# Kernel optimization log

Hardware: AMD Instinct MI355X
Metric: run time of the kernel (lower is better)

The kernel has to match this reference:

```python
import jax, jax.numpy as jnp
import numpy as np

N = 40000   # nodes
E = 600000  # edges
G = 64      # graphs
DIN = 128   # input feature dim
H = 128     # hidden_channels
L = 3       # num_layers


def setup_inputs() -> dict:
    key = jax.random.key(0)
    ks = jax.random.split(key, 16)
    s = 0.05
    inp = {}
    inp["x"] = jax.random.normal(ks[0], (N, DIN), jnp.float32)
    inp["edge_attr"] = jax.random.normal(ks[1], (E,), jnp.float32)
    inp["node_w"] = jax.random.normal(ks[2], (DIN, H), jnp.float32) * s
    inp["node_b"] = jnp.zeros((H,), jnp.float32)
    inp["edge_w"] = jax.random.normal(ks[3], (1, H), jnp.float32) * s
    inp["edge_b"] = jnp.zeros((H,), jnp.float32)
    inp["t"] = jnp.ones((L,), jnp.float32)  # learn_t init 1.0
    inp["lin1_w"] = jax.random.normal(ks[4], (L, H, 2 * H), jnp.float32) * s
    inp["lin1_b"] = jnp.zeros((L, 2 * H), jnp.float32)
    inp["ln1_g"] = jnp.ones((L, 2 * H), jnp.float32)
    inp["ln1_bt"] = jnp.zeros((L, 2 * H), jnp.float32)
    inp["lin2_w"] = jax.random.normal(ks[5], (L, 2 * H, H), jnp.float32) * s
    inp["lin2_b"] = jnp.zeros((L, H), jnp.float32)
    inp["blk_g"] = jnp.ones((L, H), jnp.float32)
    inp["blk_b"] = jnp.zeros((L, H), jnp.float32)
    inp["hw1"] = jax.random.normal(ks[6], (H, H // 2), jnp.float32) * s
    inp["hb1"] = jnp.zeros((H // 2,), jnp.float32)
    inp["hw2"] = jax.random.normal(ks[7], (H // 2, H // 4), jnp.float32) * s
    inp["hb2"] = jnp.zeros((H // 4,), jnp.float32)
    inp["hw3"] = jax.random.normal(ks[8], (H // 4, 1), jnp.float32) * s
    inp["hb3"] = jnp.zeros((1,), jnp.float32)
    inp["edge_index"] = jax.random.randint(ks[9], (2, E), 0, N, jnp.int32)
    inp["batch"] = jnp.sort(jax.random.randint(ks[10], (N,), 0, G, jnp.int32))
    return inp


def _layer_norm(v, g, b):
    mu = jnp.mean(v, axis=-1, keepdims=True)
    var = jnp.var(v, axis=-1, keepdims=True)
    return (v - mu) * jax.lax.rsqrt(var + 1e-5) * g + b


def reference(x, edge_attr, node_w, node_b, edge_w, edge_b, t,
              lin1_w, lin1_b, ln1_g, ln1_bt, lin2_w, lin2_b,
              blk_g, blk_b, hw1, hb1, hw2, hb2, hw3, hb3,
              edge_index, batch):
    src, dst = edge_index[0], edge_index[1]
    h = x @ node_w + node_b                       # [N, H]
    ea = edge_attr[:, None] @ edge_w + edge_b     # [E, H]

    def genconv(xn, i):
        # message: relu(x_j + e) + eps
        msg = jax.nn.relu(xn[src] + ea) + 1e-7    # [E, H]
        # scatter-softmax over dst with learnable temperature t
        logit = msg * t[i]
        m = jax.ops.segment_max(logit, dst, num_segments=N)
        m = jnp.where(jnp.isfinite(m), m, 0.0)    # isolated nodes
        ex = jnp.exp(logit - m[dst])
        den = jax.ops.segment_sum(ex, dst, num_segments=N)
        agg = jax.ops.segment_sum(ex * msg, dst, num_segments=N) / jnp.maximum(den, 1e-16)
        o = agg + xn                              # add root
        # GENConv MLP: Linear(H,2H) -> LayerNorm -> ReLU -> Linear(2H,H)
        o = jax.nn.relu(_layer_norm(o @ lin1_w[i] + lin1_b[i], ln1_g[i], ln1_bt[i]))
        return o @ lin2_w[i] + lin2_b[i]

    # layer 0: bare conv (as in the torch forward)
    h = genconv(h, 0)
    # layers 1..L-1: DeepGCNLayer res+ (norm -> act -> [dropout=id in eval] -> conv -> residual)
    for i in range(1, L):
        r = jax.nn.relu(_layer_norm(h, blk_g[i], blk_b[i]))
        h = h + genconv(r, i)
    # final norm+act uses layer 0's norm/act
    h = jax.nn.relu(_layer_norm(h, blk_g[0], blk_b[0]))
    # global mean pool over graphs
    cnt = jax.ops.segment_sum(jnp.ones((N,), h.dtype), batch, num_segments=G)
    pooled = jax.ops.segment_sum(h, batch, num_segments=G) / jnp.maximum(cnt, 1.0)[:, None]
    # MLP head (dropout = identity in eval)
    o = jax.nn.relu(pooled @ hw1 + hb1)
    o = jax.nn.relu(o @ hw2 + hb2)
    return o @ hw3 + hb3                          # [G, 1]
```

## Files before the change

kernel.cpp:

```cpp
#include <hip/hip_runtime.h>
#include <math.h>

#define NN 40000
#define NE 600000
#define NG 64
#define DIM_IN 128
#define HH 128
#define HH2 256

using half8 = __attribute__((ext_vector_type(8))) _Float16;
using half4 = __attribute__((ext_vector_type(4))) _Float16;
using h2    = __attribute__((ext_vector_type(2))) _Float16;
using f4    = __attribute__((ext_vector_type(4))) float;

__device__ __forceinline__ int lower_bound_dev(const int* a, int n, int key) {
    int lo = 0, hi = n;
    while (lo < hi) { int mid = (lo + hi) >> 1; if (a[mid] < key) lo = mid + 1; else hi = mid; }
    return lo;
}

#define NX (NN*DIM_IN)
#define NX4 (NX/4)
__global__ void convert_kernel(const float* __restrict__ x, const float* __restrict__ node_w,
                               const float* __restrict__ lin1_w, const float* __restrict__ lin2_w,
                               _Float16* __restrict__ xh, _Float16* __restrict__ nwt,
                               _Float16* __restrict__ w1t, _Float16* __restrict__ w2t)
{
    int id = blockIdx.x * blockDim.x + threadIdx.x;
    if (id < NX4) {
        float4 v = *(const float4*)(x + (size_t)id * 4);
        half4 o; o.x = (_Float16)v.x; o.y = (_Float16)v.y; o.z = (_Float16)v.z; o.w = (_Float16)v.w;
        *(half4*)(xh + (size_t)id * 4) = o;
        return;
    }
    id -= NX4;
    if (id < 16384) { int n = id >> 7, k = id & 127; nwt[id] = (_Float16)node_w[k*128 + n]; return; }
    id -= 16384;
    if (id < 98304) {
        int l = id >> 15, r = id & 32767;
        int n = r >> 7, k = r & 127;
        w1t[id] = (_Float16)lin1_w[l*32768 + k*256 + n];
        return;
    }
    id -= 98304;
    if (id < 98304) {
        int l = id >> 15, r = id & 32767;
        int n = r >> 8, k = r & 255;
        w2t[id] = (_Float16)lin2_w[l*32768 + k*128 + n];
    }
}

__global__ void count_rank_kernel(const int* __restrict__ dst, int* __restrict__ counts,
                                  int* __restrict__ rank) {
    int e = blockIdx.x * blockDim.x + threadIdx.x;
    if (e < NE) rank[e] = atomicAdd(&counts[dst[e]], 1);
}

__global__ __launch_bounds__(1024) void scanA_kernel(const int* __restrict__ counts,
                                                     int* __restrict__ tmp, int* __restrict__ btot) {
    __shared__ int wpre[16];
    int t = threadIdx.x, lane = t & 63, wid = t >> 6;
    int i = blockIdx.x * 1024 + t;
    int v = (i < NN) ? counts[i] : 0;
    int s = v;
    #pragma unroll
    for (int off = 1; off < 64; off <<= 1) {
        int u = __shfl_up(s, off, 64);
        if (lane >= off) s += u;
    }
    if (lane == 63) wpre[wid] = s;
    __syncthreads();
    if (t == 0) {
        int run = 0;
        #pragma unroll
        for (int j = 0; j < 16; ++j) { int xv = wpre[j]; wpre[j] = run; run += xv; }
        btot[blockIdx.x] = run;
    }
    __syncthreads();
    if (i < NN) tmp[i] = s + wpre[wid];
}

__global__ __launch_bounds__(64) void scanB_kernel(const int* __restrict__ btot,
                                                   int* __restrict__ boff, int nb) {
    int t = threadIdx.x;
    int v = (t < nb) ? btot[t] : 0;
    int s = v;
    #pragma unroll
    for (int off = 1; off < 64; off <<= 1) {
        int u = __shfl_up(s, off, 64);
        if (t >= off) s += u;
    }
    if (t < nb) boff[t] = s - v;
}

__global__ __launch_bounds__(1024) void scanC_kernel(const int* __restrict__ tmp,
                                                     const int* __restrict__ boff,
                                                     int* __restrict__ rowp) {
    int i = blockIdx.x * 1024 + threadIdx.x;
    if (i < NN) rowp[i + 1] = tmp[i] + boff[blockIdx.x];
    if (i == 0) rowp[0] = 0;
}

__global__ void fill2_kernel(const int* __restrict__ src, const int* __restrict__ dst,
                             const float* __restrict__ eattr, const int* __restrict__ rowp,
                             const int* __restrict__ rank, int2* __restrict__ rec) {
    int e = blockIdx.x * blockDim.x + threadIdx.x;
    if (e < NE) {
        int pos = rowp[dst[e]] + rank[e];
        rec[pos] = make_int2(src[e], __float_as_int(eattr[e]));
    }
}

__global__ __launch_bounds__(256) void agg_kernel(
    const _Float16* __restrict__ xh,
    const int* __restrict__ row_ptr,
    const int2* __restrict__ rec,
    const float* __restrict__ ew, const float* __restrict__ eb,
    const float* __restrict__ tptr, int layer,
    _Float16* __restrict__ oh)
{
    int d = blockIdx.x * 4 + (threadIdx.x >> 6);
    int lane = threadIdx.x & 63;
    int c0 = 2 * lane;
    float tc = tptr[layer];
    float ew0 = ew[c0], eb0 = eb[c0];
    float ew1 = ew[c0 + 1], eb1 = eb[c0 + 1];
    int beg = row_ptr[d], end = row_ptr[d + 1];
    float den0 = 0.f, num0 = 0.f, den1 = 0.f, num1 = 0.f;
    for (int base = beg; base < end; base += 64) {
        int cnt = min(64, end - base);
        int2 mv = rec[base + min(lane, cnt - 1)];
        int sv = mv.x;
        float av = __int_as_float(mv.y);
        h2 gA[8], gB[8]; float aA[8], aB[8];
        auto issue = [&](h2 (&g)[8], float (&aa)[8], int j0) {
            #pragma unroll
            for (int u = 0; u < 8; ++u) {
                int jj = min(j0 + u, cnt - 1);
                int s = __shfl(sv, jj, 64);
                aa[u] = __shfl(av, jj, 64);
                g[u] = *(const h2*)(xh + ((size_t)s << 7) + c0);
            }
        };
        auto consume = [&](h2 (&g)[8], float (&aa)[8], int j0) {
            int lim = min(8, cnt - j0);
            #pragma unroll
            for (int u = 0; u < 8; ++u) {
                if (u < lim) {
                    float m0 = fmaxf(__fmaf_rn(aa[u], ew0, eb0) + (float)g[u].x, 0.f) + 1e-7f;
                    float m1 = fmaxf(__fmaf_rn(aa[u], ew1, eb1) + (float)g[u].y, 0.f) + 1e-7f;
                    float e0 = __expf(m0 * tc), e1 = __expf(m1 * tc);
                    den0 += e0; num0 = __fmaf_rn(e0, m0, num0);
                    den1 += e1; num1 = __fmaf_rn(e1, m1, num1);
                }
            }
        };
        issue(gA, aA, 0);
        for (int j0 = 0; j0 < cnt; j0 += 16) {
            if (j0 + 8 < cnt)  issue(gB, aB, j0 + 8);
            consume(gA, aA, j0);
            if (j0 + 16 < cnt) issue(gA, aA, j0 + 16);
            if (j0 + 8 < cnt)  consume(gB, aB, j0 + 8);
        }
    }
    h2 sv2 = *(const h2*)(xh + ((size_t)d << 7) + c0);
    float o0 = num0 / fmaxf(den0, 1e-16f) + (float)sv2.x;
    float o1 = num1 / fmaxf(den1, 1e-16f) + (float)sv2.y;
    h2 ov; ov.x = (_Float16)o0; ov.y = (_Float16)o1;
    *(h2*)(oh + ((size_t)d << 7) + c0) = ov;
}

__global__ __launch_bounds__(256) void gemm_mfma(
    const _Float16* __restrict__ A, const _Float16* __restrict__ Bt,
    const float* __restrict__ bias, _Float16* __restrict__ C,
    int M, int N, int K)
{
    constexpr int LDA = 40;
    __shared__ _Float16 As[64 * LDA];
    __shared__ _Float16 Bs[128 * LDA];
    int t = threadIdx.x;
    int row0 = blockIdx.y * 64;
    int col0 = blockIdx.x * 128;
    int w = t >> 6, lane = t & 63;
    int wm = w & 1, wn = w >> 1;
    int q = lane >> 4, l16 = lane & 15;
    f4 acc[2][4];
    #pragma unroll
    for (int i = 0; i < 2; ++i)
        #pragma unroll
        for (int j = 0; j < 4; ++j)
            acc[i][j] = (f4){0.f, 0.f, 0.f, 0.f};

    for (int k0 = 0; k0 < K; k0 += 32) {
        {
            int r = t >> 2, seg = t & 3;
            *(float4*)&As[r * LDA + seg * 8] =
                *(const float4*)(A + (size_t)(row0 + r) * K + k0 + seg * 8);
        }
        #pragma unroll
        for (int i = 0; i < 2; ++i) {
            int idx = t + i * 256;
            int r = idx >> 2, seg = idx & 3;
            *(float4*)&Bs[r * LDA + seg * 8] =
                *(const float4*)(Bt + (size_t)(col0 + r) * K + k0 + seg * 8);
        }
        __syncthreads();
        half8 af[2], bf[4];
        #pragma unroll
        for (int i = 0; i < 2; ++i)
            af[i] = *(const half8*)&As[(wm * 32 + i * 16 + l16) * LDA + q * 8];
        #pragma unroll
        for (int j = 0; j < 4; ++j)
            bf[j] = *(const half8*)&Bs[(wn * 64 + j * 16 + l16) * LDA + q * 8];
        #pragma unroll
        for (int i = 0; i < 2; ++i)
            #pragma unroll
            for (int j = 0; j < 4; ++j)
                acc[i][j] = __builtin_amdgcn_mfma_f32_16x16x32_f16(af[i], bf[j], acc[i][j], 0, 0, 0);
        __syncthreads();
    }
    #pragma unroll
    for (int j = 0; j < 4; ++j) {
        int col = col0 + wn * 64 + j * 16 + l16;
        float bv = bias[col];
        #pragma unroll
        for (int i = 0; i < 2; ++i) {
            int rbase = row0 + wm * 32 + i * 16 + q * 4;
            #pragma unroll
            for (int rg = 0; rg < 4; ++rg)
                C[(size_t)(rbase + rg) * N + col] = (_Float16)(acc[i][j][rg] + bv);
        }
    }
}

template<int RES>
__global__ __launch_bounds__(256) void mlp_fused(
    const _Float16* __restrict__ Ain,
    const _Float16* __restrict__ w1t,
    const float* __restrict__ b1,
    const float* __restrict__ g1, const float* __restrict__ bt1,
    const _Float16* __restrict__ w2t,
    const float* __restrict__ b2,
    float* __restrict__ h,
    const float* __restrict__ bg, const float* __restrict__ bb,
    _Float16* __restrict__ xout)
{
    constexpr int LDA = 136;
    constexpr int LDB = 40;
    constexpr int LDM = 264;
    __shared__ _Float16 As[64 * LDA];
    __shared__ _Float16 Bs[256 * LDB];
    __shared__ _Float16 midh[64 * LDM];
    __shared__ float ssum[64][2], ssum2[64][2];
    int t = threadIdx.x;
    int row0 = blockIdx.x * 64;
    int w = t >> 6, lane = t & 63;
    int wm = w & 1, wn = w >> 1;
    int q = lane >> 4, l16 = lane & 15;

    #pragma unroll
    for (int p = 0; p < 4; ++p) {
        int idx = t + p * 256;
        int r = idx >> 4, seg = idx & 15;
        *(float4*)&As[r * LDA + seg * 8] =
            *(const float4*)(Ain + (size_t)(row0 + r) * 128 + seg * 8);
    }

    f4 acc[2][8];
    #pragma unroll
    for (int i = 0; i < 2; ++i)
        #pragma unroll
        for (int j = 0; j < 8; ++j)
            acc[i][j] = (f4){0.f, 0.f, 0.f, 0.f};
    for (int k0 = 0; k0 < 128; k0 += 32) {
        #pragma unroll
        for (int p = 0; p < 4; ++p) {
            int idx = t + p * 256;
            int r = idx >> 2, seg = idx & 3;
            *(float4*)&Bs[r * LDB + seg * 8] =
                *(const float4*)(w1t + (size_t)r * 128 + k0 + seg * 8);
        }
        __syncthreads();
        half8 af[2], bf[8];
        #pragma unroll
        for (int i = 0; i < 2; ++i)
            af[i] = *(const half8*)&As[(wm * 32 + i * 16 + l16) * LDA + k0 + q * 8];
        #pragma unroll
        for (int j = 0; j < 8; ++j)
            bf[j] = *(const half8*)&Bs[(wn * 128 + j * 16 + l16) * LDB + q * 8];
        #pragma unroll
        for (int i = 0; i < 2; ++i)
            #pragma unroll
            for (int j = 0; j < 8; ++j)
                acc[i][j] = __builtin_amdgcn_mfma_f32_16x16x32_f16(af[i], bf[j], acc[i][j], 0, 0, 0);
        __syncthreads();
    }

    float b1v[8], g1v[8], bt1v[8];
    #pragma unroll
    for (int j = 0; j < 8; ++j) {
        int col = wn * 128 + j * 16 + l16;
        b1v[j] = b1[col]; g1v[j] = g1[col]; bt1v[j] = bt1[col];
    }
    float vals[2][8][4];
    #pragma unroll
    for (int i = 0; i < 2; ++i)
        #pragma unroll
        for (int j = 0; j < 8; ++j)
            #pragma unroll
            for (int rg = 0; rg < 4; ++rg)
                vals[i][j][rg] = acc[i][j][rg] + b1v[j];
    #pragma unroll
    for (int i = 0; i < 2; ++i) {
        #pragma unroll
        for (int rg = 0; rg < 4; ++rg) {
            float ps = 0.f, ps2 = 0.f;
            #pragma unroll
            for (int j = 0; j < 8; ++j) { float v = vals[i][j][rg]; ps += v; ps2 += v * v; }
            #pragma unroll
            for (int off = 1; off < 16; off <<= 1) {
                ps  += __shfl_xor(ps,  off, 16);
                ps2 += __shfl_xor(ps2, off, 16);
            }
            if (l16 == 0) {
                int row = wm * 32 + i * 16 + q * 4 + rg;
                ssum[row][wn] = ps; ssum2[row][wn] = ps2;
            }
        }
    }
    __syncthreads();
    #pragma unroll
    for (int i = 0; i < 2; ++i) {
        #pragma unroll
        for (int rg = 0; rg < 4; ++rg) {
            int row = wm * 32 + i * 16 + q * 4 + rg;
            float S = ssum[row][0] + ssum[row][1];
            float S2 = ssum2[row][0] + ssum2[row][1];
            float mu = S * (1.0f / 256.0f);
            float var = S2 * (1.0f / 256.0f) - mu * mu;
            float rstd = rsqrtf(var + 1e-5f);
            #pragma unroll
            for (int j = 0; j < 8; ++j) {
                int col = wn * 128 + j * 16 + l16;
                float o = fmaxf((vals[i][j][rg] - mu) * rstd * g1v[j] + bt1v[j], 0.f);
                midh[row * LDM + col] = (_Float16)o;
            }
        }
    }
    __syncthreads();

    f4 acc2[2][4];
    #pragma unroll
    for (int i = 0; i < 2; ++i)
        #pragma unroll
        for (int j = 0; j < 4; ++j)
            acc2[i][j] = (f4){0.f, 0.f, 0.f, 0.f};
    for (int k0 = 0; k0 < 256; k0 += 32) {
        #pragma unroll
        for (int p = 0; p < 2; ++p) {
            int idx = t + p * 256;
            int r = idx >> 2, seg = idx & 3;
            *(float4*)&Bs[r * LDB + seg * 8] =
                *(const float4*)(w2t + (size_t)r * 256 + k0 + seg * 8);
        }
        __syncthreads();
        half8 af2[2], bf2[4];
        #pragma unroll
        for (int i = 0; i < 2; ++i)
            af2[i] = *(const half8*)&midh[(wm * 32 + i * 16 + l16) * LDM + k0 + q * 8];
        #pragma unroll
        for (int j = 0; j < 4; ++j)
            bf2[j] = *(const half8*)&Bs[(wn * 64 + j * 16 + l16) * LDB + q * 8];
        #pragma unroll
        for (int i = 0; i < 2; ++i)
            #pragma unroll
            for (int j = 0; j < 4; ++j)
                acc2[i][j] = __builtin_amdgcn_mfma_f32_16x16x32_f16(af2[i], bf2[j], acc2[i][j], 0, 0, 0);
        __syncthreads();
    }

    float b2v[4], bgv[4], bbv[4];
    #pragma unroll
    for (int j = 0; j < 4; ++j) {
        int col = wn * 64 + j * 16 + l16;
        b2v[j] = b2[col]; bgv[j] = bg[col]; bbv[j] = bb[col];
    }
    float ov[2][4][4];
    #pragma unroll
    for (int i = 0; i < 2; ++i) {
        #pragma unroll
        for (int rg = 0; rg < 4; ++rg) {
            int row = wm * 32 + i * 16 + q * 4 + rg;
            #pragma unroll
            for (int j = 0; j < 4; ++j) {
                int col = wn * 64 + j * 16 + l16;
                float v = acc2[i][j][rg] + b2v[j];
                size_t gidx = (size_t)(row0 + row) * 128 + col;
                if (RES) v += h[gidx];
                h[gidx] = v;
                ov[i][j][rg] = v;
            }
        }
    }
    #pragma unroll
    for (int i = 0; i < 2; ++i) {
        #pragma unroll
        for (int rg = 0; rg < 4; ++rg) {
            float ps = 0.f, ps2 = 0.f;
            #pragma unroll
            for (int j = 0; j < 4; ++j) { float v = ov[i][j][rg]; ps += v; ps2 += v * v; }
            #pragma unroll
            for (int off = 1; off < 16; off <<= 1) {
                ps  += __shfl_xor(ps,  off, 16);
                ps2 += __shfl_xor(ps2, off, 16);
            }
            if (l16 == 0) {
                int row = wm * 32 + i * 16 + q * 4 + rg;
                ssum[row][wn] = ps; ssum2[row][wn] = ps2;
            }
        }
    }
    __syncthreads();
    #pragma unroll
    for (int i = 0; i < 2; ++i) {
        #pragma unroll
        for (int rg = 0; rg < 4; ++rg) {
            int row = wm * 32 + i * 16 + q * 4 + rg;
            float S = ssum[row][0] + ssum[row][1];
            float S2 = ssum2[row][0] + ssum2[row][1];
            float mu = S * (1.0f / 128.0f);
            float var = S2 * (1.0f / 128.0f) - mu * mu;
            float rstd = rsqrtf(var + 1e-5f);
            #pragma unroll
            for (int j = 0; j < 4; ++j) {
                int col = wn * 64 + j * 16 + l16;
                float o = fmaxf((ov[i][j][rg] - mu) * rstd * bgv[j] + bbv[j], 0.f);
                xout[(size_t)(row0 + row) * 128 + col] = (_Float16)o;
            }
        }
    }
}

__global__ __launch_bounds__(128) void pool_kernel(
    const _Float16* __restrict__ f, const int* __restrict__ batch, float* __restrict__ pooled)
{
    int g = blockIdx.x;
    int chunk = blockIdx.y;
    int c = threadIdx.x;
    int s = lower_bound_dev(batch, NN, g);
    int e = lower_bound_dev(batch, NN, g + 1);
    int len = e - s;
    if (len <= 0) return;
    int nch = gridDim.y;
    int per = (len + nch - 1) / nch;
    int cs = s + chunk * per;
    int ce = min(cs + per, e);
    if (cs >= ce) return;
    float acc = 0.f;
    for (int n = cs; n < ce; ++n) acc += (float)f[(size_t)n * HH + c];
    atomicAdd(&pooled[g * HH + c], acc);
}

__global__ __launch_bounds__(128) void head_kernel(
    const float* __restrict__ pooled, const int* __restrict__ batch,
    const float* __restrict__ hw1, const float* __restrict__ hb1,
    const float* __restrict__ hw2, const float* __restrict__ hb2,
    const float* __restrict__ hw3, const float* __restrict__ hb3,
    float* __restrict__ out)
{
    __shared__ float p[HH];
    __shared__ float o1[64];
    __shared__ float o2[32];
    int g = blockIdx.x;
    int t = threadIdx.x;
    int s = lower_bound_dev(batch, NN, g);
    int e = lower_bound_dev(batch, NN, g + 1);
    float cnt = fmaxf((float)(e - s), 1.0f);
    p[t] = pooled[g * HH + t] / cnt;
    __syncthreads();
    if (t < 64) {
        float acc = hb1[t];
        for (int k = 0; k < HH; ++k) acc += p[k] * hw1[k * 64 + t];
        o1[t] = fmaxf(acc, 0.f);
    }
    __syncthreads();
    if (t < 32) {
        float acc = hb2[t];
        for (int k = 0; k < 64; ++k) acc += o1[k] * hw2[k * 32 + t];
        o2[t] = fmaxf(acc, 0.f);
    }
    __syncthreads();
    if (t == 0) {
        float acc = hb3[0];
        for (int k = 0; k < 32; ++k) acc += o2[k] * hw3[k];
        out[g] = acc;
    }
}

extern "C" void kernel_launch(void* const* d_in, const int* in_sizes, int n_in,
                              void* d_out, int out_size, void* d_ws, size_t ws_size,
                              hipStream_t stream)
{
    const float* x      = (const float*)d_in[0];
    const float* eattr  = (const float*)d_in[1];
    const float* node_w = (const float*)d_in[2];
    const float* node_b = (const float*)d_in[3];
    const float* edge_w = (const float*)d_in[4];
    const float* edge_b = (const float*)d_in[5];
    const float* tptr   = (const float*)d_in[6];
    const float* lin1_w = (const float*)d_in[7];
    const float* lin1_b = (const float*)d_in[8];
    const float* ln1_g  = (const float*)d_in[9];
    const float* ln1_bt = (const float*)d_in[10];
    const float* lin2_w = (const float*)d_in[11];
    const float* lin2_b = (const float*)d_in[12];
    const float* blk_g  = (const float*)d_in[13];
    const float* blk_b  = (const float*)d_in[14];
    const float* hw1    = (const float*)d_in[15];
    const float* hb1    = (const float*)d_in[16];
    const float* hw2    = (const float*)d_in[17];
    const float* hb2    = (const float*)d_in[18];
    const float* hw3    = (const float*)d_in[19];
    const float* hb3    = (const float*)d_in[20];
    const int*   eidx   = (const int*)d_in[21];
    const int*   batch  = (const int*)d_in[22];
    const int* src = eidx;
    const int* dst = eidx + NE;
    float* out = (float*)d_out;

    char* ws = (char*)d_ws;
    size_t off = 0;
    auto carve = [&](size_t bytes) -> char* {
        char* p = ws + off;
        off = (off + bytes + 255) & ~(size_t)255;
        return p;
    };
    float*    h      = (float*)carve((size_t)NN * HH * 4);
    _Float16* xh_in  = (_Float16*)carve((size_t)NX * 2);
    _Float16* xnh    = (_Float16*)carve((size_t)NN * HH * 2);
    _Float16* oh     = (_Float16*)carve((size_t)NN * HH * 2);
    _Float16* rh     = (_Float16*)carve((size_t)NN * HH * 2);
    _Float16* nwt    = (_Float16*)carve((size_t)16384 * 2);
    _Float16* w1t    = (_Float16*)carve((size_t)98304 * 2);
    _Float16* w2t    = (_Float16*)carve((size_t)98304 * 2);
    int*      counts = (int*)carve((size_t)NN * 4);
    int*      rank   = (int*)carve((size_t)NE * 4);
    int*      tmp    = (int*)carve((size_t)NN * 4);
    int*      btot   = (int*)carve((size_t)64 * 4);
    int*      boff   = (int*)carve((size_t)64 * 4);
    int*      rowp   = (int*)carve((size_t)(NN + 1) * 4);
    int2*     rec    = (int2*)carve((size_t)NE * 8);
    float*    pooled = (float*)carve((size_t)NG * HH * 4);

    hipMemsetAsync(counts, 0, (size_t)NN * 4, stream);
    hipMemsetAsync(pooled, 0, (size_t)NG * HH * 4, stream);

    {
        int total = NX4 + 16384 + 98304 + 98304;
        convert_kernel<<<(total + 255) / 256, 256, 0, stream>>>(
            x, node_w, lin1_w, lin2_w, xh_in, nwt, w1t, w2t);
    }
    const int NB = (NN + 1023) / 1024;
    count_rank_kernel<<<(NE + 255) / 256, 256, 0, stream>>>(dst, counts, rank);
    scanA_kernel<<<NB, 1024, 0, stream>>>(counts, tmp, btot);
    scanB_kernel<<<1, 64, 0, stream>>>(btot, boff, NB);
    scanC_kernel<<<NB, 1024, 0, stream>>>(tmp, boff, rowp);
    fill2_kernel<<<(NE + 255) / 256, 256, 0, stream>>>(src, dst, eattr, rowp, rank, rec);

    gemm_mfma<<<dim3(1, NN / 64), 256, 0, stream>>>(xh_in, nwt, node_b, xnh, NN, HH, DIM_IN);

    agg_kernel<<<NN / 4, 256, 0, stream>>>(xnh, rowp, rec, edge_w, edge_b, tptr, 0, oh);
    mlp_fused<0><<<NN / 64, 256, 0, stream>>>(
        oh, w1t, lin1_b, ln1_g, ln1_bt, w2t, lin2_b,
        h, blk_g + 1 * HH, blk_b + 1 * HH, xnh);
    agg_kernel<<<NN / 4, 256, 0, stream>>>(xnh, rowp, rec, edge_w, edge_b, tptr, 1, oh);
    mlp_fused<1><<<NN / 64, 256, 0, stream>>>(
        oh, w1t + 32768, lin1_b + HH2, ln1_g + HH2, ln1_bt + HH2, w2t + 32768, lin2_b + HH,
        h, blk_g + 2 * HH, blk_b + 2 * HH, xnh);
    agg_kernel<<<NN / 4, 256, 0, stream>>>(xnh, rowp, rec, edge_w, edge_b, tptr, 2, oh);
    mlp_fused<1><<<NN / 64, 256, 0, stream>>>(
        oh, w1t + 2 * 32768, lin1_b + 2 * HH2, ln1_g + 2 * HH2, ln1_bt + 2 * HH2,
        w2t + 2 * 32768, lin2_b + 2 * HH,
        h, blk_g, blk_b, rh);

    pool_kernel<<<dim3(NG, 8), 128, 0, stream>>>(rh, batch, pooled);
    head_kernel<<<NG, 128, 0, stream>>>(pooled, batch, hw1, hb1, hw2, hb2, hw3, hb3, out);
}
```

Measured before the change: 395.3 us.

## Fuse input conversion into GEMM, widen agg lanes, fuse pooling into final MLP

Removes the separate fp32-to-fp16 conversion of x by converting inside the node GEMM's A-tile load. Reworks aggregation so each lane handles 4 channels and two half-waves split edges, combined by a shuffle, and uses exp2 with a pre-scaled temperature. Fuses global mean pooling into the last MLP kernel via per-element atomics, dropping the final feature write and pool kernel. The atomics into 64 graph rows may contend heavily.

```diff
diff --git a/kernel.cpp b/kernel.cpp
--- a/kernel.cpp
+++ b/kernel.cpp
@@ -19,21 +19,12 @@
     return lo;
 }
 
-#define NX (NN*DIM_IN)
-#define NX4 (NX/4)
-__global__ void convert_kernel(const float* __restrict__ x, const float* __restrict__ node_w,
-                               const float* __restrict__ lin1_w, const float* __restrict__ lin2_w,
-                               _Float16* __restrict__ xh, _Float16* __restrict__ nwt,
-                               _Float16* __restrict__ w1t, _Float16* __restrict__ w2t)
+__global__ void convert_w_kernel(const float* __restrict__ node_w,
+                                 const float* __restrict__ lin1_w, const float* __restrict__ lin2_w,
+                                 _Float16* __restrict__ nwt,
+                                 _Float16* __restrict__ w1t, _Float16* __restrict__ w2t)
 {
     int id = blockIdx.x * blockDim.x + threadIdx.x;
-    if (id < NX4) {
-        float4 v = *(const float4*)(x + (size_t)id * 4);
-        half4 o; o.x = (_Float16)v.x; o.y = (_Float16)v.y; o.z = (_Float16)v.z; o.w = (_Float16)v.w;
-        *(half4*)(xh + (size_t)id * 4) = o;
-        return;
-    }
-    id -= NX4;
     if (id < 16384) { int n = id >> 7, k = id & 127; nwt[id] = (_Float16)node_w[k*128 + n]; return; }
     id -= 16384;
     if (id < 98304) {
@@ -121,57 +112,73 @@
 {
     int d = blockIdx.x * 4 + (threadIdx.x >> 6);
     int lane = threadIdx.x & 63;
-    int c0 = 2 * lane;
-    float tc = tptr[layer];
-    float ew0 = ew[c0], eb0 = eb[c0];
-    float ew1 = ew[c0 + 1], eb1 = eb[c0 + 1];
+    int half = lane >> 5;
+    int sl = lane & 31;
+    int c0 = 4 * sl;
+    float tc2 = tptr[layer] * 1.44269504f;
+    float ewv[4], ebv[4];
+    #pragma unroll
+    for (int c = 0; c < 4; ++c) { ewv[c] = ew[c0 + c]; ebv[c] = eb[c0 + c]; }
     int beg = row_ptr[d], end = row_ptr[d + 1];
-    float den0 = 0.f, num0 = 0.f, den1 = 0.f, num1 = 0.f;
+    float den[4] = {0.f, 0.f, 0.f, 0.f}, num[4] = {0.f, 0.f, 0.f, 0.f};
     for (int base = beg; base < end; base += 64) {
         int cnt = min(64, end - base);
         int2 mv = rec[base + min(lane, cnt - 1)];
         int sv = mv.x;
         float av = __int_as_float(mv.y);
-        h2 gA[8], gB[8]; float aA[8], aB[8];
-        auto issue = [&](h2 (&g)[8], float (&aa)[8], int j0) {
-            #pragma unroll
-            for (int u = 0; u < 8; ++u) {
-                int jj = min(j0 + u, cnt - 1);
-                int s = __shfl(sv, jj, 64);
-                aa[u] = __shfl(av, jj, 64);
-                g[u] = *(const h2*)(xh + ((size_t)s << 7) + c0);
+        int pcnt = (cnt + 1) >> 1;
+        half4 gA[4], gB[4]; float aA[4], aB[4];
+        auto issue = [&](half4 (&g)[4], float (&aa)[4], int p0) {
+            #pragma unroll
+            for (int u = 0; u < 4; ++u) {
+                int je = min(2 * (p0 + u) + half, cnt - 1);
+                int s = __shfl(sv, je, 64);
+                aa[u] = __shfl(av, je, 64);
+                g[u] = *(const half4*)(xh + ((size_t)s << 7) + c0);
             }
         };
-        auto consume = [&](h2 (&g)[8], float (&aa)[8], int j0) {
-            int lim = min(8, cnt - j0);
-            #pragma unroll
-            for (int u = 0; u < 8; ++u) {
-                if (u < lim) {
-                    float m0 = fmaxf(__fmaf_rn(aa[u], ew0, eb0) + (float)g[u].x, 0.f) + 1e-7f;
-                    float m1 = fmaxf(__fmaf_rn(aa[u], ew1, eb1) + (float)g[u].y, 0.f) + 1e-7f;
-                    float e0 = __expf(m0 * tc), e1 = __expf(m1 * tc);
-                    den0 += e0; num0 = __fmaf_rn(e0, m0, num0);
-                    den1 += e1; num1 = __fmaf_rn(e1, m1, num1);
+        auto consume = [&](half4 (&g)[4], float (&aa)[4], int p0) {
+            #pragma unroll
+            for (int u = 0; u < 4; ++u) {
+                int je = 2 * (p0 + u) + half;
+                if (je < cnt) {
+                    #pragma unroll
+                    for (int c = 0; c < 4; ++c) {
+                        float r = fmaxf(__fmaf_rn(aa[u], ewv[c], ebv[c]) + (float)g[u][c], 0.f);
+                        float e = exp2f(r * tc2);
+                        den[c] += e;
+                        num[c] = __fmaf_rn(e, r, num[c]);
+                    }
                 }
             }
         };
         issue(gA, aA, 0);
-        for (int j0 = 0; j0 < cnt; j0 += 16) {
-            if (j0 + 8 < cnt)  issue(gB, aB, j0 + 8);
-            consume(gA, aA, j0);
-            if (j0 + 16 < cnt) issue(gA, aA, j0 + 16);
-            if (j0 + 8 < cnt)  consume(gB, aB, j0 + 8);
-        }
-    }
-    h2 sv2 = *(const h2*)(xh + ((size_t)d << 7) + c0);
-    float o0 = num0 / fmaxf(den0, 1e-16f) + (float)sv2.x;
-    float o1 = num1 / fmaxf(den1, 1e-16f) + (float)sv2.y;
-    h2 ov; ov.x = (_Float16)o0; ov.y = (_Float16)o1;
-    *(h2*)(oh + ((size_t)d << 7) + c0) = ov;
+        for (int p0 = 0; p0 < pcnt; p0 += 8) {
+            if (p0 + 4 < pcnt) issue(gB, aB, p0 + 4);
+            consume(gA, aA, p0);
+            if (p0 + 8 < pcnt) issue(gA, aA, p0 + 8);
+            if (p0 + 4 < pcnt) consume(gB, aB, p0 + 4);
+        }
+    }
+    #pragma unroll
+    for (int c = 0; c < 4; ++c) {
+        den[c] += __shfl_xor(den[c], 32, 64);
+        num[c] += __shfl_xor(num[c], 32, 64);
+    }
+    if (half == 0) {
+        half4 sv4 = *(const half4*)(xh + ((size_t)d << 7) + c0);
+        half4 ov;
+        #pragma unroll
+        for (int c = 0; c < 4; ++c) {
+            float o = num[c] / fmaxf(den[c], 1e-16f) + 1e-7f + (float)sv4[c];
+            ov[c] = (_Float16)o;
+        }
+        *(half4*)(oh + ((size_t)d << 7) + c0) = ov;
+    }
 }
 
 __global__ __launch_bounds__(256) void gemm_mfma(
-    const _Float16* __restrict__ A, const _Float16* __restrict__ Bt,
+    const float* __restrict__ A, const _Float16* __restrict__ Bt,
     const float* __restrict__ bias, _Float16* __restrict__ C,
     int M, int N, int K)
 {
@@ -192,10 +199,13 @@
             acc[i][j] = (f4){0.f, 0.f, 0.f, 0.f};
 
     for (int k0 = 0; k0 < K; k0 += 32) {
-        {
-            int r = t >> 2, seg = t & 3;
-            *(float4*)&As[r * LDA + seg * 8] =
-                *(const float4*)(A + (size_t)(row0 + r) * K + k0 + seg * 8);
+        #pragma unroll
+        for (int p = 0; p < 2; ++p) {
+            int idx = t + p * 256;
+            int r = idx >> 3, seg = idx & 7;
+            float4 v = *(const float4*)(A + (size_t)(row0 + r) * K + k0 + seg * 4);
+            half4 o; o.x = (_Float16)v.x; o.y = (_Float16)v.y; o.z = (_Float16)v.z; o.w = (_Float16)v.w;
+            *(half4*)&As[r * LDA + seg * 4] = o;
         }
         #pragma unroll
         for (int i = 0; i < 2; ++i) {
@@ -233,7 +243,7 @@
     }
 }
 
-template<int RES>
+template<int RES, int FINAL>
 __global__ __launch_bounds__(256) void mlp_fused(
     const _Float16* __restrict__ Ain,
     const _Float16* __restrict__ w1t,
@@ -243,7 +253,8 @@
     const float* __restrict__ b2,
     float* __restrict__ h,
     const float* __restrict__ bg, const float* __restrict__ bb,
-    _Float16* __restrict__ xout)
+    _Float16* __restrict__ xout,
+    const int* __restrict__ batch, float* __restrict__ pooled)
 {
     constexpr int LDA = 136;
     constexpr int LDB = 40;
@@ -385,6 +396,14 @@
         int col = wn * 64 + j * 16 + l16;
         b2v[j] = b2[col]; bgv[j] = bg[col]; bbv[j] = bb[col];
     }
+    int gidv[2][4];
+    if (FINAL) {
+        #pragma unroll
+        for (int i = 0; i < 2; ++i)
+            #pragma unroll
+            for (int rg = 0; rg < 4; ++rg)
+                gidv[i][rg] = batch[row0 + wm * 32 + i * 16 + q * 4 + rg];
+    }
     float ov[2][4][4];
     #pragma unroll
     for (int i = 0; i < 2; ++i) {
@@ -397,7 +416,7 @@
                 float v = acc2[i][j][rg] + b2v[j];
                 size_t gidx = (size_t)(row0 + row) * 128 + col;
                 if (RES) v += h[gidx];
-                h[gidx] = v;
+                if (!FINAL) h[gidx] = v;
                 ov[i][j][rg] = v;
             }
         }
@@ -435,30 +454,13 @@
             for (int j = 0; j < 4; ++j) {
                 int col = wn * 64 + j * 16 + l16;
                 float o = fmaxf((ov[i][j][rg] - mu) * rstd * bgv[j] + bbv[j], 0.f);
-                xout[(size_t)(row0 + row) * 128 + col] = (_Float16)o;
-            }
-        }
-    }
-}
-
-__global__ __launch_bounds__(128) void pool_kernel(
-    const _Float16* __restrict__ f, const int* __restrict__ batch, float* __restrict__ pooled)
-{
-    int g = blockIdx.x;
-    int chunk = blockIdx.y;
-    int c = threadIdx.x;
-    int s = lower_bound_dev(batch, NN, g);
-    int e = lower_bound_dev(batch, NN, g + 1);
-    int len = e - s;
-    if (len <= 0) return;
-    int nch = gridDim.y;
-    int per = (len + nch - 1) / nch;
-    int cs = s + chunk * per;
-    int ce = min(cs + per, e);
-    if (cs >= ce) return;
-    float acc = 0.f;
-    for (int n = cs; n < ce; ++n) acc += (float)f[(size_t)n * HH + c];
-    atomicAdd(&pooled[g * HH + c], acc);
+                if (!FINAL)
+                    xout[(size_t)(row0 + row) * 128 + col] = (_Float16)o;
+                else
+                    atomicAdd(&pooled[gidv[i][rg] * HH + col], o);
+            }
+        }
+    }
 }
 
 __global__ __launch_bounds__(128) void head_kernel(
@@ -536,10 +538,8 @@
         return p;
     };
     float*    h      = (float*)carve((size_t)NN * HH * 4);
-    _Float16* xh_in  = (_Float16*)carve((size_t)NX * 2);
     _Float16* xnh    = (_Float16*)carve((size_t)NN * HH * 2);
     _Float16* oh     = (_Float16*)carve((size_t)NN * HH * 2);
-    _Float16* rh     = (_Float16*)carve((size_t)NN * HH * 2);
     _Float16* nwt    = (_Float16*)carve((size_t)16384 * 2);
     _Float16* w1t    = (_Float16*)carve((size_t)98304 * 2);
     _Float16* w2t    = (_Float16*)carve((size_t)98304 * 2);
@@ -556,9 +556,9 @@
     hipMemsetAsync(pooled, 0, (size_t)NG * HH * 4, stream);
 
     {
-        int total = NX4 + 16384 + 98304 + 98304;
-        convert_kernel<<<(total + 255) / 256, 256, 0, stream>>>(
-            x, node_w, lin1_w, lin2_w, xh_in, nwt, w1t, w2t);
+        int total = 16384 + 98304 + 98304;
+        convert_w_kernel<<<(total + 255) / 256, 256, 0, stream>>>(
+            node_w, lin1_w, lin2_w, nwt, w1t, w2t);
     }
     const int NB = (NN + 1023) / 1024;
     count_rank_kernel<<<(NE + 255) / 256, 256, 0, stream>>>(dst, counts, rank);
@@ -567,22 +567,21 @@
     scanC_kernel<<<NB, 1024, 0, stream>>>(tmp, boff, rowp);
     fill2_kernel<<<(NE + 255) / 256, 256, 0, stream>>>(src, dst, eattr, rowp, rank, rec);
 
-    gemm_mfma<<<dim3(1, NN / 64), 256, 0, stream>>>(xh_in, nwt, node_b, xnh, NN, HH, DIM_IN);
+    gemm_mfma<<<dim3(1, NN / 64), 256, 0, stream>>>(x, nwt, node_b, xnh, NN, HH, DIM_IN);
 
     agg_kernel<<<NN / 4, 256, 0, stream>>>(xnh, rowp, rec, edge_w, edge_b, tptr, 0, oh);
-    mlp_fused<0><<<NN / 64, 256, 0, stream>>>(
+    mlp_fused<0, 0><<<NN / 64, 256, 0, stream>>>(
         oh, w1t, lin1_b, ln1_g, ln1_bt, w2t, lin2_b,
-        h, blk_g + 1 * HH, blk_b + 1 * HH, xnh);
+        h, blk_g + 1 * HH, blk_b + 1 * HH, xnh, nullptr, nullptr);
     agg_kernel<<<NN / 4, 256, 0, stream>>>(xnh, rowp, rec, edge_w, edge_b, tptr, 1, oh);
-    mlp_fused<1><<<NN / 64, 256, 0, stream>>>(
+    mlp_fused<1, 0><<<NN / 64, 256, 0, stream>>>(
         oh, w1t + 32768, lin1_b + HH2, ln1_g + HH2, ln1_bt + HH2, w2t + 32768, lin2_b + HH,
-        h, blk_g + 2 * HH, blk_b + 2 * HH, xnh);
+        h, blk_g + 2 * HH, blk_b + 2 * HH, xnh, nullptr, nullptr);
     agg_kernel<<<NN / 4, 256, 0, stream>>>(xnh, rowp, rec, edge_w, edge_b, tptr, 2, oh);
-    mlp_fused<1><<<NN / 64, 256, 0, stream>>>(
+    mlp_fused<1, 1><<<NN / 64, 256, 0, stream>>>(
         oh, w1t + 2 * 32768, lin1_b + 2 * HH2, ln1_g + 2 * HH2, ln1_bt + 2 * HH2,
         w2t + 2 * 32768, lin2_b + 2 * HH,
-        h, blk_g, blk_b, rh);
-
-    pool_kernel<<<dim3(NG, 8), 128, 0, stream>>>(rh, batch, pooled);
+        h, blk_g, blk_b, nullptr, batch, pooled);
+
     head_kernel<<<NG, 128, 0, stream>>>(pooled, batch, hw1, hb1, hw2, hb2, hw3, hb3, out);
 }
```

After: 496.0 us. 1.25x slower.
